# Performance work log

Hardware: AMD Instinct MI355X
Metric: run time of the kernel (lower is better)

Reference implementation:

```python
import jax, jax.numpy as jnp
import numpy as np
import math

DIM = 2048
N_HEADS = 16
HEAD_DIM = DIM // N_HEADS
B, S = 2, 2048
EPS = 1e-6


def rms_norm(x, w):
    return x * jax.lax.rsqrt(jnp.mean(x * x, axis=-1, keepdims=True) + EPS) * w


def rotate(x, cos, sin):
    x1, x2 = jnp.split(x, 2, axis=-1)
    rotated = jnp.concatenate((-x2, x1), axis=-1)
    return x * cos + rotated * sin


def setup_inputs() -> dict:
    key = jax.random.key(0)
    ks = jax.random.split(key, 16)
    half = HEAD_DIM // 2
    inv_freq = 1.0 / (10000.0 ** (jnp.arange(0, half, dtype=jnp.float32) / half))
    t = jnp.arange(S, dtype=jnp.float32)
    freqs = jnp.einsum('s,d->sd', t, inv_freq)
    emb = jnp.concatenate((freqs, freqs), axis=-1)  # [S, HEAD_DIM]
    cos = jnp.cos(emb)[None, None]  # [1,1,S,HEAD_DIM]
    sin = jnp.sin(emb)[None, None]
    # causal additive mask [1,1,S,S]
    causal = jnp.triu(jnp.full((S, S), -1e9, dtype=jnp.float32), k=1)[None, None]
    sc = 0.02
    return {
        'x': jax.random.normal(ks[0], (B, S, DIM), jnp.float32),
        'cos': cos,
        'sin': sin,
        'mask': causal,
        'attn_norm_w': jnp.ones((DIM,), jnp.float32),
        'ffn_norm_w': jnp.ones((DIM,), jnp.float32),
        'wq': jax.random.normal(ks[1], (DIM, DIM), jnp.float32) * sc,
        'wk': jax.random.normal(ks[2], (DIM, DIM), jnp.float32) * sc,
        'wv': jax.random.normal(ks[3], (DIM, DIM), jnp.float32) * sc,
        'wo': jax.random.normal(ks[4], (DIM, DIM), jnp.float32) * sc,
        'w1': jax.random.normal(ks[5], (DIM, 4 * DIM), jnp.float32) * sc,
        'w2': jax.random.normal(ks[6], (4 * DIM, DIM), jnp.float32) * sc,
        'w3': jax.random.normal(ks[7], (DIM, 4 * DIM), jnp.float32) * sc,
    }


def reference(x, cos, sin, mask, attn_norm_w, ffn_norm_w, wq, wk, wv, wo, w1, w2, w3):
    b, s, d = x.shape
    h = rms_norm(x, attn_norm_w)
    q = (h @ wq).reshape(b, s, N_HEADS, HEAD_DIM).transpose(0, 2, 1, 3)
    k = (h @ wk).reshape(b, s, N_HEADS, HEAD_DIM).transpose(0, 2, 1, 3)
    v = (h @ wv).reshape(b, s, N_HEADS, HEAD_DIM).transpose(0, 2, 1, 3)
    q = rotate(q, cos, sin)
    k = rotate(k, cos, sin)
    attn = jnp.einsum('bhqd,bhkd->bhqk', q, k) / math.sqrt(HEAD_DIM)
    attn = attn + mask
    attn = jax.nn.softmax(attn, axis=-1)
    out = jnp.einsum('bhqk,bhkd->bhqd', attn, v)
    out = out.transpose(0, 2, 1, 3).reshape(b, s, d)
    x = x + out @ wo
    h = rms_norm(x, ffn_norm_w)
    x = x + (jax.nn.silu(h @ w1) * (h @ w3)) @ w2
    return x
```

## Files before the change

kernel.cpp:

```cpp
#include <hip/hip_runtime.h>

#define DIM 2048
#define HDIM 128
#define NH 16
#define SEQ 2048
#define BATCH 2
#define MROWS (BATCH*SEQ)
#define QKP 6144

typedef __attribute__((ext_vector_type(8))) short short8;
typedef __attribute__((ext_vector_type(4))) float f32x4;

template<int N> struct ic { static constexpr int value = N; };

__device__ __forceinline__ unsigned short f2bf(float f) {
  union { float f; unsigned u; } v; v.f = f;
  unsigned r = v.u + 0x7FFFu + ((v.u >> 16) & 1u);
  return (unsigned short)(r >> 16);
}
__device__ __forceinline__ float bf2f(unsigned short b) {
  union { unsigned u; float f; } v; v.u = ((unsigned)b) << 16;
  return v.f;
}

__device__ __forceinline__ void gload16(const void* g, void* l) {
  __builtin_amdgcn_global_load_lds((const __attribute__((address_space(1))) unsigned int*)g,
                                   (__attribute__((address_space(3))) unsigned int*)l,
                                   16, 0, 0);
}

__global__ __launch_bounds__(256) void rmsnorm_kernel(const float* __restrict__ x,
                                                      const float* __restrict__ w,
                                                      unsigned short* __restrict__ out) {
  const int row = blockIdx.x;
  const int t = threadIdx.x;
  const float* xr = x + (size_t)row * DIM;
  float4 v0 = ((const float4*)xr)[t*2];
  float4 v1 = ((const float4*)xr)[t*2+1];
  float ss = v0.x*v0.x + v0.y*v0.y + v0.z*v0.z + v0.w*v0.w
           + v1.x*v1.x + v1.y*v1.y + v1.z*v1.z + v1.w*v1.w;
  #pragma unroll
  for (int i = 1; i < 64; i <<= 1) ss += __shfl_xor(ss, i);
  __shared__ float red[4];
  if ((t & 63) == 0) red[t >> 6] = ss;
  __syncthreads();
  float sum = red[0] + red[1] + red[2] + red[3];
  float sc = rsqrtf(sum * (1.0f/DIM) + 1e-6f);
  const float* wr = w + t*8;
  unsigned short ob[8];
  ob[0] = f2bf(v0.x*sc*wr[0]); ob[1] = f2bf(v0.y*sc*wr[1]);
  ob[2] = f2bf(v0.z*sc*wr[2]); ob[3] = f2bf(v0.w*sc*wr[3]);
  ob[4] = f2bf(v1.x*sc*wr[4]); ob[5] = f2bf(v1.y*sc*wr[5]);
  ob[6] = f2bf(v1.z*sc*wr[6]); ob[7] = f2bf(v1.w*sc*wr[7]);
  uint4 pk;
  pk.x = (unsigned)ob[0] | ((unsigned)ob[1] << 16);
  pk.y = (unsigned)ob[2] | ((unsigned)ob[3] << 16);
  pk.z = (unsigned)ob[4] | ((unsigned)ob[5] << 16);
  pk.w = (unsigned)ob[6] | ((unsigned)ob[7] << 16);
  *((uint4*)(out + (size_t)row*DIM + t*8)) = pk;
}

__global__ __launch_bounds__(256) void transpose_w_kernel(const float* __restrict__ W,
                                                          unsigned short* __restrict__ Wt,
                                                          int K, int N) {
  __shared__ float tile[32][33];
  const int k0 = blockIdx.x*32, n0 = blockIdx.y*32;
  const int tx = threadIdx.x, ty = threadIdx.y;
  #pragma unroll
  for (int i=0;i<4;i++) tile[ty+i*8][tx] = W[(size_t)(k0+ty+i*8)*N + n0+tx];
  __syncthreads();
  #pragma unroll
  for (int i=0;i<4;i++) Wt[(size_t)(n0+ty+i*8)*K + k0+tx] = f2bf(tile[tx][ty+i*8]);
}

__global__ __launch_bounds__(256) void transpose_v_kernel(const unsigned short* __restrict__ v,
                                                          int vpitch,
                                                          unsigned short* __restrict__ vt) {
  __shared__ unsigned short tile[32][33];
  const int b = blockIdx.z;
  const int s0 = blockIdx.x*32, c0 = blockIdx.y*32;
  const int tx = threadIdx.x, ty = threadIdx.y;
  #pragma unroll
  for (int i=0;i<4;i++) tile[ty+i*8][tx] = v[((size_t)(b*SEQ + s0+ty+i*8))*vpitch + c0+tx];
  __syncthreads();
  #pragma unroll
  for (int i=0;i<4;i++) vt[((size_t)(b*DIM + c0+ty+i*8))*SEQ + s0+tx] = tile[tx][ty+i*8];
}

__global__ __launch_bounds__(256) void rope_qk(unsigned short* __restrict__ qk,
                                               const float* __restrict__ cosb,
                                               const float* __restrict__ sinb) {
  const size_t idx = (size_t)blockIdx.x * 256 + threadIdx.x;
  const int d = (int)(idx & 63);
  const int h = (int)((idx >> 6) & 31);
  const int row = (int)(idx >> 11);
  const int s = row & (SEQ-1);
  const size_t base = (size_t)row * QKP + h*HDIM + d;
  float a  = bf2f(qk[base]);
  float bq = bf2f(qk[base+64]);
  float c1 = cosb[s*HDIM + d],    s1 = sinb[s*HDIM + d];
  float c2 = cosb[s*HDIM + d+64], s2 = sinb[s*HDIM + d+64];
  qk[base]    = f2bf(a*c1 - bq*s1);
  qk[base+64] = f2bf(bq*c2 + a*s2);
}

template<int BM, int EPI>
__global__ __launch_bounds__(512, 2) void gemm_pipe(const unsigned short* __restrict__ A,
                                                    const unsigned short* __restrict__ Bt,
                                                    const float* __restrict__ aux,
                                                    void* __restrict__ outp,
                                                    int M, int N, int K) {
  constexpr int HRA = BM/2;
  constexpr int MF  = BM/32;
  constexpr int APP = MF/4;
  constexpr int LA  = BM/128;
  constexpr int AHS = HRA*64;
  constexpr int BB  = 4*AHS;
  extern __shared__ unsigned short ldsd[];
  const int tid = threadIdx.x, l = tid & 63, wid = tid >> 6;
  const int wm = wid >> 2, wn = wid & 3;
  const int lr = l & 15, lg = l >> 4;
  const int bh = wn >> 1, brow0 = (wn & 1)*64;

  const int nbx = N >> 8;
  const int SW = (nbx >= 8) ? (nbx >> 3) : 1;
  const int xcd = (int)blockIdx.x & 7;
  const int ii  = (int)blockIdx.x >> 3;
  const int by = ii / SW;
  const int bx = xcd * SW + (ii % SW);
  const int m0 = by * BM, n0 = bx * 256;

  const int m7 = lr & 7;
  const int jks0 = ((lg    ) ^ m7) << 3;
  const int jks1 = ((4 + lg) ^ m7) << 3;
  const unsigned short* ldsA0 = ldsd + wm*AHS + lr*64;
  const unsigned short* ldsA1 = ldsA0 + 2*AHS;
  const unsigned short* ldsB0 = ldsd + BB + bh*8192 + (brow0+lr)*64;
  const unsigned short* ldsB1 = ldsB0 + 2*8192;

  const int r0 = tid >> 3;
  const int jsw = ((tid & 7) ^ (r0 & 7)) << 3;
  const unsigned short* srcA[2][LA];
  #pragma unroll
  for (int h=0;h<2;h++)
    #pragma unroll
    for (int c=0;c<LA;c++)
      srcA[h][c] = A + (size_t)(m0 + h*HRA + c*64 + r0)*K + jsw;
  const unsigned short* srcB[2][2];
  #pragma unroll
  for (int h=0;h<2;h++)
    #pragma unroll
    for (int c=0;c<2;c++)
      srcB[h][c] = Bt + (size_t)(n0 + h*128 + c*64 + r0)*K + jsw;
  unsigned short* dstL = ldsd + tid*8;

  int kO = 0;
  auto stA = [&](int db, int half, int tiled) {
    #pragma unroll
    for (int c=0;c<LA;c++)
      gload16(srcA[half][c] + kO + tiled, dstL + (db*2+half)*AHS + c*4096);
  };
  auto stB = [&](int db, int half, int tiled) {
    #pragma unroll
    for (int c=0;c<2;c++)
      gload16(srcB[half][c] + kO + tiled, dstL + BB + (db*2+half)*8192 + c*4096);
  };

  f32x4 acc[MF][4] = {};
  short8 bfrag[4][2];
  const int ntile = K >> 6;

  stB(0,0,0); stB(0,1,0);
  stA(0,0,0); stA(0,1,0);
  stB(1,0,64); stB(1,1,64);
  asm volatile("s_waitcnt vmcnt(4)" ::: "memory");
  __builtin_amdgcn_sched_barrier(0);
  __builtin_amdgcn_s_barrier();

  auto phase = [&](auto PC, auto LC) {
    constexpr int P = decltype(PC)::value;
    constexpr int LAST = decltype(LC)::value;
    constexpr int hi = P >> 2;
    constexpr int p  = P & 3;
    if constexpr (p == 0) {
      const unsigned short* bB = hi ? ldsB1 : ldsB0;
      #pragma unroll
      for (int nf=0;nf<4;nf++) {
        bfrag[nf][0] = *(const short8*)(bB + nf*1024 + jks0);
        bfrag[nf][1] = *(const short8*)(bB + nf*1024 + jks1);
      }
    }
    const unsigned short* aB = hi ? ldsA1 : ldsA0;
    short8 afr[APP][2];
    #pragma unroll
    for (int mi=0;mi<APP;mi++) {
      afr[mi][0] = *(const short8*)(aB + (p*APP+mi)*1024 + jks0);
      afr[mi][1] = *(const short8*)(aB + (p*APP+mi)*1024 + jks1);
    }
    if constexpr (P == 0)      stA(1, 0, 64);
    else if constexpr (P == 1) stA(1, 1, 64);
    else if constexpr (!LAST) {
      if constexpr (P == 2)      stB(0, 0, 128);
      else if constexpr (P == 3) stB(0, 1, 128);
      else if constexpr (P == 4) stA(0, 0, 128);
      else if constexpr (P == 5) stA(0, 1, 128);
      else if constexpr (P == 6) stB(1, 0, 192);
      else if constexpr (P == 7) stB(1, 1, 192);
    }
    if constexpr (p == 0) {
      asm volatile("s_waitcnt lgkmcnt(8)" ::: "memory");
    }
    if constexpr (P == 3) {
      if constexpr (LAST) { asm volatile("s_waitcnt vmcnt(0)" ::: "memory"); }
      else                { asm volatile("s_waitcnt vmcnt(4)" ::: "memory"); }
    }
    if constexpr (P == 7 && !LAST) {
      asm volatile("s_waitcnt vmcnt(4)" ::: "memory");
    }
    __builtin_amdgcn_s_barrier();
    asm volatile("s_waitcnt lgkmcnt(0)" ::: "memory");
    __builtin_amdgcn_sched_barrier(0);
    __builtin_amdgcn_s_setprio(1);
    #pragma unroll
    for (int mi=0;mi<APP;mi++)
      #pragma unroll
      for (int nf=0;nf<4;nf++)
        #pragma unroll
        for (int ks=0;ks<2;ks++)
          acc[p*APP+mi][nf] = __builtin_amdgcn_mfma_f32_16x16x32_bf16(afr[mi][ks], bfrag[nf][ks], acc[p*APP+mi][nf], 0,0,0);
    __builtin_amdgcn_s_setprio(0);
    __builtin_amdgcn_s_barrier();
  };

  for (int T = 0; T + 2 < ntile; T += 2, kO += 128) {
    phase(ic<0>{}, ic<0>{}); phase(ic<1>{}, ic<0>{});
    phase(ic<2>{}, ic<0>{}); phase(ic<3>{}, ic<0>{});
    phase(ic<4>{}, ic<0>{}); phase(ic<5>{}, ic<0>{});
    phase(ic<6>{}, ic<0>{}); phase(ic<7>{}, ic<0>{});
  }
  phase(ic<0>{}, ic<1>{}); phase(ic<1>{}, ic<1>{});
  phase(ic<2>{}, ic<1>{}); phase(ic<3>{}, ic<1>{});
  phase(ic<4>{}, ic<1>{}); phase(ic<5>{}, ic<1>{});
  phase(ic<6>{}, ic<1>{}); phase(ic<7>{}, ic<1>{});

  #pragma unroll
  for (int mf = 0; mf < MF; mf++)
    #pragma unroll
    for (int nf = 0; nf < 4; nf++)
      #pragma unroll
      for (int r = 0; r < 4; r++) {
        const int row = m0 + wm*HRA + mf*16 + lg*4 + r;
        const int col = n0 + wn*64 + nf*16 + lr;
        const size_t idx = (size_t)row * N + col;
        if constexpr (EPI == 0) {
          ((unsigned short*)outp)[idx] = f2bf(acc[mf][nf][r]);
        } else if constexpr (EPI == 1) {
          ((float*)outp)[idx] = acc[mf][nf][r] + aux[idx];
        } else {
          float g = acc[mf][nf][r];
          float u = bf2f(((unsigned short*)outp)[idx]);
          float sg = u / (1.0f + __expf(-u));
          ((unsigned short*)outp)[idx] = f2bf(sg * g);
        }
      }
}

__global__ __launch_bounds__(256, 2) void attn_kernel(const unsigned short* __restrict__ q,
                                                      const unsigned short* __restrict__ k,
                                                      const unsigned short* __restrict__ vt,
                                                      unsigned short* __restrict__ ao) {
  const int t = threadIdx.x, lane = t & 63, w = t >> 6;
  const int qt = (int)gridDim.x - 1 - (int)blockIdx.x;
  const int bh = blockIdx.y;
  const int b = bh >> 4, h = bh & 15;
  const int lr = lane & 15, lg = lane >> 4;
  const int q0w = qt*128 + w*32;

  __shared__ __attribute__((aligned(16))) unsigned short Kb[64*128];
  __shared__ __attribute__((aligned(16))) unsigned short Vb[128*64];
  __shared__ __attribute__((aligned(16))) unsigned short Ones[16*72];
  __shared__ __attribute__((aligned(16))) unsigned short P[4][32*72];
  unsigned short* pw = &P[w][0];

  for (int idx = t; idx < 16*72; idx += 256) Ones[idx] = (idx < 72) ? 0x3F80 : 0;

  short8 aq[2][4];
  {
    const unsigned short* qp = q + ((size_t)(b*SEQ + q0w + lr))*QKP + h*HDIM;
    #pragma unroll
    for (int mf=0;mf<2;mf++)
      #pragma unroll
      for (int c=0;c<4;c++) aq[mf][c] = *(const short8*)(qp + (size_t)mf*16*QKP + c*32 + lg*8);
  }

  f32x4 accO[2][8] = {};
  f32x4 accO9[2] = {};
  float mrow[2][4];
  #pragma unroll
  for (int mf=0;mf<2;mf++)
    #pragma unroll
    for (int r=0;r<4;r++) mrow[mf][r] = -3.0e38f;

  const float scale = 0.08838834764831845f;
  const unsigned short* kg = k + (size_t)(b*SEQ)*QKP + h*HDIM;
  const unsigned short* vg = vt + (size_t)(bh*HDIM)*SEQ;

  const unsigned short* kga[4]; const unsigned short* vga[4];
  unsigned short* kld[4]; unsigned short* vld[4];
  #pragma unroll
  for (int i=0;i<4;i++) {
    const int D = i*256 + t;
    const int rk = D >> 4, jk = D & 15;
    kga[i] = kg + (size_t)rk*QKP + ((jk ^ (rk & 7)) * 8);
    const int rv = D >> 3, jv = D & 7;
    vga[i] = vg + (size_t)rv*SEQ + ((jv ^ (rv & 7)) * 8);
    kld[i] = &Kb[i*2048 + w*512];
    vld[i] = &Vb[i*2048 + w*512];
  }

  const int KV_END = qt*128 + 128;

  for (int kv0 = 0; kv0 < KV_END; kv0 += 64) {
    #pragma unroll
    for (int i=0;i<4;i++) gload16(kga[i] + (size_t)kv0*QKP, kld[i]);
    #pragma unroll
    for (int i=0;i<4;i++) gload16(vga[i] + kv0, vld[i]);
    __syncthreads();

    if (kv0 < q0w + 32) {
      f32x4 sc[2][4] = {};
      #pragma unroll
      for (int blk=0;blk<4;blk++) {
        const int krow = blk*16 + lr;
        const int sw = (krow & 7) << 3;
        #pragma unroll
        for (int c=0;c<4;c++) {
          short8 bk = *(const short8*)&Kb[krow*128 + ((c*32 + lg*8) ^ sw)];
          sc[0][blk] = __builtin_amdgcn_mfma_f32_16x16x32_bf16(aq[0][c], bk, sc[0][blk], 0,0,0);
          sc[1][blk] = __builtin_amdgcn_mfma_f32_16x16x32_bf16(aq[1][c], bk, sc[1][blk], 0,0,0);
        }
      }
      #pragma unroll
      for (int mf=0;mf<2;mf++)
        #pragma unroll
        for (int blk=0;blk<4;blk++)
          #pragma unroll
          for (int r=0;r<4;r++) sc[mf][blk][r] *= scale;
      if (kv0 + 63 > q0w) {
        #pragma unroll
        for (int mf=0;mf<2;mf++)
          #pragma unroll
          for (int blk=0;blk<4;blk++)
            #pragma unroll
            for (int r=0;r<4;r++)
              if (kv0 + blk*16 + lr > q0w + mf*16 + lg*4 + r) sc[mf][blk][r] = -1.0e30f;
      }
      float pm[2][4];
      #pragma unroll
      for (int mf=0;mf<2;mf++)
        #pragma unroll
        for (int r=0;r<4;r++) {
          float m0 = fmaxf(fmaxf(sc[mf][0][r], sc[mf][1][r]), fmaxf(sc[mf][2][r], sc[mf][3][r]));
          #pragma unroll
          for (int x=1;x<16;x<<=1) m0 = fmaxf(m0, __shfl_xor(m0, x));
          pm[mf][r] = m0;
        }
      int need = 0;
      #pragma unroll
      for (int mf=0;mf<2;mf++)
        #pragma unroll
        for (int r=0;r<4;r++) need |= (pm[mf][r] > mrow[mf][r] + 8.0f) ? 1 : 0;
      if (__any(need)) {
        #pragma unroll
        for (int mf=0;mf<2;mf++)
          #pragma unroll
          for (int r=0;r<4;r++) {
            const float mn = fmaxf(mrow[mf][r], pm[mf][r]);
            const float fc = __expf(mrow[mf][r] - mn);
            mrow[mf][r] = mn;
            #pragma unroll
            for (int n=0;n<8;n++) accO[mf][n][r] *= fc;
            accO9[mf][r] *= fc;
          }
      }
      #pragma unroll
      for (int mf=0;mf<2;mf++)
        #pragma unroll
        for (int blk=0;blk<4;blk++)
          #pragma unroll
          for (int r=0;r<4;r++) {
            const float p = __expf(sc[mf][blk][r] - mrow[mf][r]);
            pw[(mf*16 + lg*4 + r)*72 + blk*16 + lr] = f2bf(p);
          }
      short8 ap[2][2];
      #pragma unroll
      for (int mf=0;mf<2;mf++)
        #pragma unroll
        for (int ks=0;ks<2;ks++) ap[mf][ks] = *(const short8*)&pw[(mf*16 + lr)*72 + ks*32 + lg*8];
      #pragma unroll
      for (int n=0;n<8;n++) {
        #pragma unroll
        for (int ks=0;ks<2;ks++) {
          const int vrow = n*16 + lr;
          const int sw = (vrow & 7) << 3;
          short8 bv = *(const short8*)&Vb[vrow*64 + ((ks*32 + lg*8) ^ sw)];
          accO[0][n] = __builtin_amdgcn_mfma_f32_16x16x32_bf16(ap[0][ks], bv, accO[0][n], 0,0,0);
          accO[1][n] = __builtin_amdgcn_mfma_f32_16x16x32_bf16(ap[1][ks], bv, accO[1][n], 0,0,0);
        }
      }
      #pragma unroll
      for (int ks=0;ks<2;ks++) {
        short8 bv9 = *(const short8*)&Ones[lr*72 + ks*32 + lg*8];
        accO9[0] = __builtin_amdgcn_mfma_f32_16x16x32_bf16(ap[0][ks], bv9, accO9[0], 0,0,0);
        accO9[1] = __builtin_amdgcn_mfma_f32_16x16x32_bf16(ap[1][ks], bv9, accO9[1], 0,0,0);
      }
    }
    __syncthreads();
  }

  #pragma unroll
  for (int mf=0;mf<2;mf++)
    #pragma unroll
    for (int r=0;r<4;r++) {
      const float lv = __shfl(accO9[mf][r], lane & 48);
      const float inv = 1.0f / lv;
      const size_t row = (size_t)(b*SEQ + q0w + mf*16 + lg*4 + r);
      #pragma unroll
      for (int n=0;n<8;n++)
        ao[row*DIM + h*HDIM + n*16 + lr] = f2bf(accO[mf][n][r] * inv);
    }
}

extern "C" void kernel_launch(void* const* d_in, const int* in_sizes, int n_in,
                              void* d_out, int out_size, void* d_ws, size_t ws_size,
                              hipStream_t stream) {
  (void)in_sizes; (void)n_in; (void)out_size; (void)ws_size;
  const float* x    = (const float*)d_in[0];
  const float* cosb = (const float*)d_in[1];
  const float* sinb = (const float*)d_in[2];
  const float* anw  = (const float*)d_in[4];
  const float* fnw  = (const float*)d_in[5];
  const float* wq   = (const float*)d_in[6];
  const float* wk   = (const float*)d_in[7];
  const float* wv   = (const float*)d_in[8];
  const float* wo   = (const float*)d_in[9];
  const float* w1   = (const float*)d_in[10];
  const float* w2   = (const float*)d_in[11];
  const float* w3   = (const float*)d_in[12];

  char* ws = (char*)d_ws;
  const size_t MB = 1048576;
  unsigned short* h     = (unsigned short*)(ws);
  unsigned short* qkvb  = (unsigned short*)(ws + 16*MB);
  unsigned short* mid   = qkvb;
  unsigned short* aob   = (unsigned short*)(ws + 67*MB);
  char* wt              = ws + 84*MB;
  unsigned short* wqkvT = (unsigned short*)wt;
  unsigned short* vtb   = (unsigned short*)wt;
  unsigned short* woT   = (unsigned short*)wt;
  unsigned short* wfT   = (unsigned short*)wt;
  float* x1f = (float*)d_out;

  dim3 b256(256);
  dim3 tb(32, 8);
  constexpr unsigned LDS256 = 131072;
  constexpr unsigned LDS128 = 98304;

  rmsnorm_kernel<<<dim3(MROWS), b256, 0, stream>>>(x, anw, h);

  transpose_w_kernel<<<dim3(64,64), tb, 0, stream>>>(wq, wqkvT,           2048, 2048);
  transpose_w_kernel<<<dim3(64,64), tb, 0, stream>>>(wk, wqkvT + 4194304, 2048, 2048);
  transpose_w_kernel<<<dim3(64,64), tb, 0, stream>>>(wv, wqkvT + 8388608, 2048, 2048);

  gemm_pipe<256,0><<<dim3(384), dim3(512), LDS256, stream>>>(h, wqkvT, nullptr, qkvb, MROWS, 6144, 2048);

  rope_qk<<<dim3(32768), b256, 0, stream>>>(qkvb, cosb, sinb);

  transpose_v_kernel<<<dim3(64,64,2), tb, 0, stream>>>(qkvb + 4096, QKP, vtb);

  attn_kernel<<<dim3(16,32), b256, 0, stream>>>(qkvb, qkvb + 2048, vtb, aob);

  transpose_w_kernel<<<dim3(64,64), tb, 0, stream>>>(wo, woT, 2048, 2048);
  gemm_pipe<128,1><<<dim3(256), dim3(512), LDS128, stream>>>(aob, woT, x, x1f, MROWS, 2048, 2048);

  rmsnorm_kernel<<<dim3(MROWS), b256, 0, stream>>>(x1f, fnw, h);

  transpose_w_kernel<<<dim3(64,256), tb, 0, stream>>>(w1, wfT, 2048, 8192);
  gemm_pipe<256,0><<<dim3(512), dim3(512), LDS256, stream>>>(h, wfT, nullptr, mid, MROWS, 8192, 2048);
  transpose_w_kernel<<<dim3(64,256), tb, 0, stream>>>(w3, wfT, 2048, 8192);
  gemm_pipe<256,3><<<dim3(512), dim3(512), LDS256, stream>>>(h, wfT, nullptr, mid, MROWS, 8192, 2048);

  transpose_w_kernel<<<dim3(256,64), tb, 0, stream>>>(w2, wfT, 8192, 2048);
  gemm_pipe<128,1><<<dim3(256), dim3(512), LDS128, stream>>>(mid, wfT, x1f, (float*)d_out, MROWS, 2048, 8192);
}
```

Baseline: 840.7 us.

## Batch weight transposes into a vectorized kernel and use a 128x128 GEMM for N=2048

Replaces the per-weight 32x32 transpose with a 64x64-tile kernel that uses float4 loads and packed bf16 stores, and handles several weights per launch through blockIdx.z. w1 and w3 are now transposed together into separate buffers. The two N=2048 GEMMs (wo and w2) switch from the 512-thread pipelined gemm_pipe<128> to a new simple 256-thread 128x128 kernel with XCD-aware block swizzle and 3 blocks per CU. That kernel is single-buffered with no load/compute overlap, so the occupancy gain may not make up for the lost pipelining.

Measured after the change: 880.7 us. 1.05x slower.

```diff
diff --git a/kernel.cpp b/kernel.cpp
--- a/kernel.cpp
+++ b/kernel.cpp
@@ -60,17 +60,34 @@
   *((uint4*)(out + (size_t)row*DIM + t*8)) = pk;
 }
 
-__global__ __launch_bounds__(256) void transpose_w_kernel(const float* __restrict__ W,
-                                                          unsigned short* __restrict__ Wt,
-                                                          int K, int N) {
-  __shared__ float tile[32][33];
-  const int k0 = blockIdx.x*32, n0 = blockIdx.y*32;
-  const int tx = threadIdx.x, ty = threadIdx.y;
-  #pragma unroll
-  for (int i=0;i<4;i++) tile[ty+i*8][tx] = W[(size_t)(k0+ty+i*8)*N + n0+tx];
+__global__ __launch_bounds__(256) void transpose3_kernel(const float* __restrict__ W0,
+                                                         const float* __restrict__ W1,
+                                                         const float* __restrict__ W2,
+                                                         unsigned short* __restrict__ D0,
+                                                         unsigned short* __restrict__ D1,
+                                                         unsigned short* __restrict__ D2,
+                                                         int K, int N) {
+  const float* W = blockIdx.z == 0 ? W0 : (blockIdx.z == 1 ? W1 : W2);
+  unsigned short* D = blockIdx.z == 0 ? D0 : (blockIdx.z == 1 ? D1 : D2);
+  __shared__ float tile[64][65];
+  const int k0 = blockIdx.x*64, n0 = blockIdx.y*64;
+  const int t = threadIdx.x;
+  const int rr = t >> 4, cc = (t & 15) * 4;
+  #pragma unroll
+  for (int i=0;i<4;i++) {
+    float4 v = *(const float4*)&W[(size_t)(k0 + rr + i*16)*N + n0 + cc];
+    tile[rr+i*16][cc] = v.x; tile[rr+i*16][cc+1] = v.y;
+    tile[rr+i*16][cc+2] = v.z; tile[rr+i*16][cc+3] = v.w;
+  }
   __syncthreads();
   #pragma unroll
-  for (int i=0;i<4;i++) Wt[(size_t)(n0+ty+i*8)*K + k0+tx] = f2bf(tile[tx][ty+i*8]);
+  for (int j=0;j<4;j++) {
+    const int n = rr + j*16;
+    uint2 pk;
+    pk.x = (unsigned)f2bf(tile[cc  ][n]) | ((unsigned)f2bf(tile[cc+1][n]) << 16);
+    pk.y = (unsigned)f2bf(tile[cc+2][n]) | ((unsigned)f2bf(tile[cc+3][n]) << 16);
+    *(uint2*)&D[(size_t)(n0 + n)*K + k0 + cc] = pk;
+  }
 }
 
 __global__ __launch_bounds__(256) void transpose_v_kernel(const unsigned short* __restrict__ v,
@@ -79,7 +96,7 @@
   __shared__ unsigned short tile[32][33];
   const int b = blockIdx.z;
   const int s0 = blockIdx.x*32, c0 = blockIdx.y*32;
-  const int tx = threadIdx.x, ty = threadIdx.y;
+  const int tx = threadIdx.x & 31, ty = threadIdx.x >> 5;
   #pragma unroll
   for (int i=0;i<4;i++) tile[ty+i*8][tx] = v[((size_t)(b*SEQ + s0+ty+i*8))*vpitch + c0+tx];
   __syncthreads();
@@ -265,6 +282,88 @@
       }
 }
 
+template<int EPI>
+__global__ __launch_bounds__(256, 3) void gemm_m97(const unsigned short* __restrict__ A,
+                                                   const unsigned short* __restrict__ Bt,
+                                                   const float* __restrict__ aux,
+                                                   void* __restrict__ outp,
+                                                   int M, int N, int K) {
+  __shared__ unsigned short As[128*32];
+  __shared__ unsigned short Bs[128*32];
+  const int tid = threadIdx.x, l = tid & 63, w = tid >> 6;
+  const int wr = w >> 1, wc = w & 1;
+  const int lr = l & 15, lg = l >> 4;
+
+  const int nbx = N >> 7;
+  const int SW = ((nbx & 7) == 0) ? (nbx >> 3) : 1;
+  const int xcd = (int)blockIdx.x & 7;
+  const int ii  = (int)blockIdx.x >> 3;
+  const int by = ii / SW;
+  const int bx = xcd * SW + (ii % SW);
+  const int m0 = by * 128, n0 = bx * 128;
+
+  const int srow = tid >> 2;
+  const int jsw = ((tid & 3) ^ (srow & 3)) << 3;
+  const unsigned short* srcA[2];
+  const unsigned short* srcB[2];
+  #pragma unroll
+  for (int c=0;c<2;c++) {
+    srcA[c] = A  + (size_t)(m0 + c*64 + srow)*K + jsw;
+    srcB[c] = Bt + (size_t)(n0 + c*64 + srow)*K + jsw;
+  }
+  unsigned short* dstA = As + tid*8;
+  unsigned short* dstB = Bs + tid*8;
+
+  const int jc = ((lg ^ (lr & 3)) << 3);
+  const unsigned short* ldsA = As + (wr*64 + lr)*32 + jc;
+  const unsigned short* ldsB = Bs + (wc*64 + lr)*32 + jc;
+
+  f32x4 acc[4][4] = {};
+  const int ntile = K >> 5;
+  int kO = 0;
+
+  for (int t = 0; t < ntile; ++t, kO += 32) {
+    #pragma unroll
+    for (int c=0;c<2;c++) {
+      gload16(srcA[c] + kO, dstA + c*2048);
+      gload16(srcB[c] + kO, dstB + c*2048);
+    }
+    __syncthreads();
+    short8 af[4], bf[4];
+    #pragma unroll
+    for (int mf=0;mf<4;mf++) af[mf] = *(const short8*)(ldsA + mf*512);
+    #pragma unroll
+    for (int nf=0;nf<4;nf++) bf[nf] = *(const short8*)(ldsB + nf*512);
+    #pragma unroll
+    for (int mf=0;mf<4;mf++)
+      #pragma unroll
+      for (int nf=0;nf<4;nf++)
+        acc[mf][nf] = __builtin_amdgcn_mfma_f32_16x16x32_bf16(af[mf], bf[nf], acc[mf][nf], 0,0,0);
+    __syncthreads();
+  }
+
+  #pragma unroll
+  for (int mf = 0; mf < 4; mf++)
+    #pragma unroll
+    for (int nf = 0; nf < 4; nf++)
+      #pragma unroll
+      for (int r = 0; r < 4; r++) {
+        const int row = m0 + wr*64 + mf*16 + lg*4 + r;
+        const int col = n0 + wc*64 + nf*16 + lr;
+        const size_t idx = (size_t)row * N + col;
+        if constexpr (EPI == 0) {
+          ((unsigned short*)outp)[idx] = f2bf(acc[mf][nf][r]);
+        } else if constexpr (EPI == 1) {
+          ((float*)outp)[idx] = acc[mf][nf][r] + aux[idx];
+        } else {
+          float g = acc[mf][nf][r];
+          float u = bf2f(((unsigned short*)outp)[idx]);
+          float sg = u / (1.0f + __expf(-u));
+          ((unsigned short*)outp)[idx] = f2bf(sg * g);
+        }
+      }
+}
+
 __global__ __launch_bounds__(256, 2) void attn_kernel(const unsigned short* __restrict__ q,
                                                       const unsigned short* __restrict__ k,
                                                       const unsigned short* __restrict__ vt,
@@ -458,38 +557,39 @@
   unsigned short* wqkvT = (unsigned short*)wt;
   unsigned short* vtb   = (unsigned short*)wt;
   unsigned short* woT   = (unsigned short*)wt;
-  unsigned short* wfT   = (unsigned short*)wt;
+  unsigned short* w1T   = (unsigned short*)wt;
+  unsigned short* w3T   = (unsigned short*)(wt + 32*MB);
+  unsigned short* w2T   = (unsigned short*)wt;
   float* x1f = (float*)d_out;
 
   dim3 b256(256);
-  dim3 tb(32, 8);
   constexpr unsigned LDS256 = 131072;
-  constexpr unsigned LDS128 = 98304;
 
   rmsnorm_kernel<<<dim3(MROWS), b256, 0, stream>>>(x, anw, h);
 
-  transpose_w_kernel<<<dim3(64,64), tb, 0, stream>>>(wq, wqkvT,           2048, 2048);
-  transpose_w_kernel<<<dim3(64,64), tb, 0, stream>>>(wk, wqkvT + 4194304, 2048, 2048);
-  transpose_w_kernel<<<dim3(64,64), tb, 0, stream>>>(wv, wqkvT + 8388608, 2048, 2048);
+  transpose3_kernel<<<dim3(32,32,3), b256, 0, stream>>>(wq, wk, wv,
+      wqkvT, wqkvT + 4194304, wqkvT + 8388608, 2048, 2048);
 
   gemm_pipe<256,0><<<dim3(384), dim3(512), LDS256, stream>>>(h, wqkvT, nullptr, qkvb, MROWS, 6144, 2048);
 
   rope_qk<<<dim3(32768), b256, 0, stream>>>(qkvb, cosb, sinb);
 
-  transpose_v_kernel<<<dim3(64,64,2), tb, 0, stream>>>(qkvb + 4096, QKP, vtb);
+  transpose_v_kernel<<<dim3(64,64,2), b256, 0, stream>>>(qkvb + 4096, QKP, vtb);
 
   attn_kernel<<<dim3(16,32), b256, 0, stream>>>(qkvb, qkvb + 2048, vtb, aob);
 
-  transpose_w_kernel<<<dim3(64,64), tb, 0, stream>>>(wo, woT, 2048, 2048);
-  gemm_pipe<128,1><<<dim3(256), dim3(512), LDS128, stream>>>(aob, woT, x, x1f, MROWS, 2048, 2048);
+  transpose3_kernel<<<dim3(32,32,1), b256, 0, stream>>>(wo, nullptr, nullptr,
+      woT, nullptr, nullptr, 2048, 2048);
+  gemm_m97<1><<<dim3(512), b256, 0, stream>>>(aob, woT, x, x1f, MROWS, 2048, 2048);
 
   rmsnorm_kernel<<<dim3(MROWS), b256, 0, stream>>>(x1f, fnw, h);
 
-  transpose_w_kernel<<<dim3(64,256), tb, 0, stream>>>(w1, wfT, 2048, 8192);
-  gemm_pipe<256,0><<<dim3(512), dim3(512), LDS256, stream>>>(h, wfT, nullptr, mid, MROWS, 8192, 2048);
-  transpose_w_kernel<<<dim3(64,256), tb, 0, stream>>>(w3, wfT, 2048, 8192);
-  gemm_pipe<256,3><<<dim3(512), dim3(512), LDS256, stream>>>(h, wfT, nullptr, mid, MROWS, 8192, 2048);
-
-  transpose_w_kernel<<<dim3(256,64), tb, 0, stream>>>(w2, wfT, 8192, 2048);
-  gemm_pipe<128,1><<<dim3(256), dim3(512), LDS128, stream>>>(mid, wfT, x1f, (float*)d_out, MROWS, 2048, 8192);
-}
+  transpose3_kernel<<<dim3(32,128,2), b256, 0, stream>>>(w1, w3, nullptr,
+      w1T, w3T, nullptr, 2048, 8192);
+  gemm_pipe<256,0><<<dim3(512), dim3(512), LDS256, stream>>>(h, w1T, nullptr, mid, MROWS, 8192, 2048);
+  gemm_pipe<256,3><<<dim3(512), dim3(512), LDS256, stream>>>(h, w3T, nullptr, mid, MROWS, 8192, 2048);
+
+  transpose3_kernel<<<dim3(128,32,1), b256, 0, stream>>>(w2, nullptr, nullptr,
+      w2T, nullptr, nullptr, 8192, 2048);
+  gemm_m97<1><<<dim3(512), b256, 0, stream>>>(mid, w2T, x1f, (float*)d_out, MROWS, 2048, 8192);
+}
```
